# Performance work log

Measured on AMD Instinct MI355X. Metric: run time of the kernel, lower is better.

## Reference

```python
import jax, jax.numpy as jnp
import numpy as np

EMPTY = -1  # sentinel for empty (vertex, region) slots, as in the TF layer


def setup_inputs() -> dict:
    key = jax.random.key(0)
    m, vertices, regions = 128, 2048, 32
    # values in [-1, vertices): -1 marks an empty slot, otherwise a vertex id
    mapping = jax.random.randint(key, (m, vertices, regions), EMPTY, vertices, dtype=jnp.int32)
    return {"mapping": mapping}


def reference(mapping):
    """Faithful JAX version of Graph2Col.call.

    TF's tf.where(mask) emits coordinates of True entries in row-major order
    with a data-dependent row count. For jit-compatibility we emit a
    fixed-size [m*V*R, ...] result where valid entries come first (same
    row-major order as tf.where) and padding rows are filled with -1.
    """
    m, V, R = mapping.shape
    total = m * V * R
    flat_map = mapping.reshape(-1)                 # [total]
    # row index is never -1, so the reduce_all mask is simply mapping != -1
    flat_mask = flat_map != EMPTY                  # [total] bool

    # stable stream compaction: valid entries first, preserving row-major order
    order = jnp.argsort(~flat_mask)                # stable sort -> tf.where ordering
    valid = flat_mask[order]                       # [total] bool

    rows = order // (V * R)
    rem = order % (V * R)
    verts = rem // R
    regs = rem % R

    # column_indices: coordinates of non-empty slots (tf.where returns int64)
    column_indices = jnp.stack([rows, verts, regs], axis=-1).astype(jnp.int64)  # [total, 3]
    # nodes_indices: (batch_row, vertex_id) gathered at those coordinates (int32)
    nodes_indices = jnp.stack([rows.astype(jnp.int32), flat_map[order]], axis=-1)  # [total, 2]

    column_indices = jnp.where(valid[:, None], column_indices, jnp.int64(EMPTY))
    nodes_indices = jnp.where(valid[:, None], nodes_indices, jnp.int32(EMPTY))
    return nodes_indices, column_indices
```

## Files before the change

### kernel.cpp

```cpp
#include <hip/hip_runtime.h>


#define EMPTY_V (-1)

constexpr int M_DIM = 128;
constexpr int V_DIM = 2048;
constexpr int R_DIM = 32;
constexpr int TOTAL = M_DIM * V_DIM * R_DIM;
constexpr int BLOCK = 256;
constexpr int CHUNK = 8192;
constexpr int NB = TOTAL / CHUNK;
constexpr int SUBT = CHUNK / (BLOCK * 4);
constexpr int NWAVE = BLOCK / 64;
constexpr int STAGE = BLOCK * 4;

__global__ __launch_bounds__(BLOCK) void k_count(const int* __restrict__ in,
                                                 int* __restrict__ counts) {
    const int b = blockIdx.x;
    const int tid = threadIdx.x;
    const int4* p = (const int4*)(in + (size_t)b * CHUNK);
    int c = 0;
#pragma unroll
    for (int s = 0; s < SUBT; ++s) {
        int4 v = p[s * BLOCK + tid];
        c += (v.x != EMPTY_V) + (v.y != EMPTY_V) + (v.z != EMPTY_V) + (v.w != EMPTY_V);
    }
    for (int d = 32; d > 0; d >>= 1) c += __shfl_down(c, d, 64);
    __shared__ int ws[NWAVE];
    const int lane = tid & 63, wid = tid >> 6;
    if (lane == 0) ws[wid] = c;
    __syncthreads();
    if (tid == 0) {
        int t = 0;
        for (int w = 0; w < NWAVE; ++w) t += ws[w];
        counts[b] = t;
    }
}

__global__ __launch_bounds__(NB) void k_scan(const int* __restrict__ counts,
                                             int* __restrict__ offsets,
                                             int* __restrict__ total_valid) {
    const int tid = threadIdx.x;
    const int lane = tid & 63, wid = tid >> 6;
    int c = counts[tid];
    int incl = c;
    for (int d = 1; d < 64; d <<= 1) {
        int y = __shfl_up(incl, d, 64);
        if (lane >= d) incl += y;
    }
    __shared__ int ws[NB / 64];
    if (lane == 63) ws[wid] = incl;
    __syncthreads();
    int woff = 0;
    for (int w = 0; w < wid; ++w) woff += ws[w];
    offsets[tid] = woff + incl - c;
    if (tid == NB - 1) *total_valid = woff + incl;
}

__global__ __launch_bounds__(BLOCK) void k_scatter(const int* __restrict__ in,
                                                   const int* __restrict__ offsets,
                                                   int* __restrict__ out_nodes,
                                                   int* __restrict__ out_cols) {
    const int b = blockIdx.x;
    const int tid = threadIdx.x;
    const int lane = tid & 63, wid = tid >> 6;
    const unsigned long long below = lane ? ((~0ull) >> (64 - lane)) : 0ull;
    __shared__ int wsum[NWAVE];
    __shared__ int s_val[STAGE];
    __shared__ int s_pos[STAGE];
    const int row = b >> 3;
    int running = offsets[b];
    const int4* p = (const int4*)(in + (size_t)b * CHUNK);
#pragma unroll 1
    for (int s = 0; s < SUBT; ++s) {
        const int4 v = p[s * BLOCK + tid];
        const int f0 = (v.x != EMPTY_V), f1 = (v.y != EMPTY_V);
        const int f2 = (v.z != EMPTY_V), f3 = (v.w != EMPTY_V);
        const unsigned long long b0 = __ballot(f0), b1 = __ballot(f1);
        const unsigned long long b2 = __ballot(f2), b3 = __ballot(f3);
        const int pre = __popcll(b0 & below) + __popcll(b1 & below) +
                        __popcll(b2 & below) + __popcll(b3 & below);
        const int wtot = __popcll(b0) + __popcll(b1) + __popcll(b2) + __popcll(b3);
        if (lane == 0) wsum[wid] = wtot;
        __syncthreads();
        int woff = 0, cnt = 0;
        for (int w = 0; w < NWAVE; ++w) {
            const int x = wsum[w];
            cnt += x;
            if (w < wid) woff += x;
        }
        int lp = woff + pre;
        const int rem0 = ((b & 7) << 13) + (s << 10) + (tid << 2);
        const int vals[4] = {v.x, v.y, v.z, v.w};
        const int fl[4] = {f0, f1, f2, f3};
#pragma unroll
        for (int j = 0; j < 4; ++j) {
            if (fl[j]) { s_val[lp] = vals[j]; s_pos[lp] = rem0 + j; ++lp; }
        }
        __syncthreads();
        int2* ndst2 = (int2*)(out_nodes + 2 * (size_t)running);
        for (int k = tid; k < cnt; k += BLOCK) {
            ndst2[k] = make_int2(row, s_val[k]);
        }
        int* cdst = out_cols + 3 * (size_t)running;
        const int cdw = 3 * cnt;
        for (int d = tid; d < cdw; d += BLOCK) {
            const int e = d / 3;
            const int r = d - 3 * e;
            int val = row;
            if (r != 0) {
                const int pp = s_pos[e];
                val = (r == 1) ? (pp >> 5) : (pp & 31);
            }
            cdst[d] = val;
        }
        running += cnt;
        __syncthreads();
    }
}

__global__ __launch_bounds__(BLOCK) void k_tail(const int* __restrict__ total_valid,
                                                int* __restrict__ out_nodes,
                                                int* __restrict__ out_cols) {
    const int tv = *total_valid;
    const int stride = gridDim.x * blockDim.x;
    for (int pos = tv + blockIdx.x * blockDim.x + threadIdx.x; pos < TOTAL;
         pos += stride) {
        out_nodes[2 * pos]     = EMPTY_V;
        out_nodes[2 * pos + 1] = EMPTY_V;
        out_cols[3 * pos]      = EMPTY_V;
        out_cols[3 * pos + 1]  = EMPTY_V;
        out_cols[3 * pos + 2]  = EMPTY_V;
    }
}

extern "C" void kernel_launch(void* const* d_in, const int* in_sizes, int n_in,
                              void* d_out, int out_size, void* d_ws, size_t ws_size,
                              hipStream_t stream) {
    const int* in = (const int*)d_in[0];
    int* out = (int*)d_out;
    int* out_nodes = out;
    int* out_cols = out + 2 * (size_t)TOTAL;
    int* ws = (int*)d_ws;
    int* counts = ws;
    int* offsets = ws + NB;
    int* tv = ws + 2 * NB;

    k_count<<<NB, BLOCK, 0, stream>>>(in, counts);
    k_scan<<<1, NB, 0, stream>>>(counts, offsets, tv);
    k_scatter<<<NB, BLOCK, 0, stream>>>(in, offsets, out_nodes, out_cols);
    k_tail<<<512, BLOCK, 0, stream>>>(tv, out_nodes, out_cols);
}
```

Measured before the change: 196.7 us.

## Fold scan and tail fill into scatter kernel, vectorize output stores

Result: faster. 192.0 us (-2.4%).

```diff
diff --git a/kernel.cpp b/kernel.cpp
--- a/kernel.cpp
+++ b/kernel.cpp
@@ -37,39 +37,40 @@
     }
 }
 
-__global__ __launch_bounds__(NB) void k_scan(const int* __restrict__ counts,
-                                             int* __restrict__ offsets,
-                                             int* __restrict__ total_valid) {
-    const int tid = threadIdx.x;
-    const int lane = tid & 63, wid = tid >> 6;
-    int c = counts[tid];
-    int incl = c;
-    for (int d = 1; d < 64; d <<= 1) {
-        int y = __shfl_up(incl, d, 64);
-        if (lane >= d) incl += y;
-    }
-    __shared__ int ws[NB / 64];
-    if (lane == 63) ws[wid] = incl;
-    __syncthreads();
-    int woff = 0;
-    for (int w = 0; w < wid; ++w) woff += ws[w];
-    offsets[tid] = woff + incl - c;
-    if (tid == NB - 1) *total_valid = woff + incl;
-}
-
 __global__ __launch_bounds__(BLOCK) void k_scatter(const int* __restrict__ in,
-                                                   const int* __restrict__ offsets,
+                                                   const int* __restrict__ counts,
                                                    int* __restrict__ out_nodes,
                                                    int* __restrict__ out_cols) {
     const int b = blockIdx.x;
     const int tid = threadIdx.x;
     const int lane = tid & 63, wid = tid >> 6;
     const unsigned long long below = lane ? ((~0ull) >> (64 - lane)) : 0ull;
+
+    __shared__ int red[2 * NWAVE];
+    {
+        const int4 c4 = ((const int4*)counts)[tid];
+        const int idx0 = tid * 4;
+        const int cs[4] = {c4.x, c4.y, c4.z, c4.w};
+        int pa = 0, ta = 0;
+#pragma unroll
+        for (int j = 0; j < 4; ++j) {
+            ta += cs[j];
+            if (idx0 + j < b) pa += cs[j];
+        }
+        for (int d = 32; d > 0; d >>= 1) {
+            pa += __shfl_down(pa, d, 64);
+            ta += __shfl_down(ta, d, 64);
+        }
+        if (lane == 0) { red[wid] = pa; red[NWAVE + wid] = ta; }
+    }
+    __syncthreads();
+    int running = 0, tv = 0;
+    for (int w = 0; w < NWAVE; ++w) { running += red[w]; tv += red[NWAVE + w]; }
+
     __shared__ int wsum[NWAVE];
     __shared__ int s_val[STAGE];
     __shared__ int s_pos[STAGE];
     const int row = b >> 3;
-    int running = offsets[b];
     const int4* p = (const int4*)(in + (size_t)b * CHUNK);
 #pragma unroll 1
     for (int s = 0; s < SUBT; ++s) {
@@ -98,34 +99,62 @@
             if (fl[j]) { s_val[lp] = vals[j]; s_pos[lp] = rem0 + j; ++lp; }
         }
         __syncthreads();
-        int2* ndst2 = (int2*)(out_nodes + 2 * (size_t)running);
-        for (int k = tid; k < cnt; k += BLOCK) {
-            ndst2[k] = make_int2(row, s_val[k]);
+
+        {
+            int2* b2p = (int2*)out_nodes + running;
+            const int head = ((running & 1) && cnt > 0) ? 1 : 0;
+            if (head && tid == 0) b2p[0] = make_int2(row, s_val[0]);
+            const int nPairs = (cnt - head) >> 1;
+            int4* b4p = (int4*)(b2p + head);
+            for (int k = tid; k < nPairs; k += BLOCK) {
+                const int e = head + 2 * k;
+                b4p[k] = make_int4(row, s_val[e], row, s_val[e + 1]);
+            }
+            if (((cnt - head) & 1) && tid == BLOCK - 1)
+                b2p[cnt - 1] = make_int2(row, s_val[cnt - 1]);
         }
-        int* cdst = out_cols + 3 * (size_t)running;
-        const int cdw = 3 * cnt;
-        for (int d = tid; d < cdw; d += BLOCK) {
-            const int e = d / 3;
-            const int r = d - 3 * e;
-            int val = row;
-            if (r != 0) {
-                const int pp = s_pos[e];
-                val = (r == 1) ? (pp >> 5) : (pp & 31);
+        {
+            int* cd = out_cols + 3 * (size_t)running;
+            const int cdw = 3 * cnt;
+            const int mis = (3 * running) & 3;
+            int peel = mis ? (4 - mis) : 0;
+            if (peel > cdw) peel = cdw;
+            if (tid < peel) {
+                const int ld = tid;
+                const int e = ld / 3, r = ld - 3 * e;
+                int vv = row;
+                if (r) { const int pp = s_pos[e]; vv = (r == 1) ? (pp >> 5) : (pp & 31); }
+                cd[ld] = vv;
             }
-            cdst[d] = val;
+            const int body = (cdw - peel) >> 2;
+            int4* c4p = (int4*)(cd + peel);
+            for (int k = tid; k < body; k += BLOCK) {
+                const int ld0 = peel + 4 * k;
+                int vv[4];
+#pragma unroll
+                for (int i = 0; i < 4; ++i) {
+                    const int ld = ld0 + i;
+                    const int e = ld / 3, r = ld - 3 * e;
+                    int x = row;
+                    if (r) { const int pp = s_pos[e]; x = (r == 1) ? (pp >> 5) : (pp & 31); }
+                    vv[i] = x;
+                }
+                c4p[k] = make_int4(vv[0], vv[1], vv[2], vv[3]);
+            }
+            const int tails = cdw - peel - 4 * body;
+            if (tid < tails) {
+                const int ld = peel + 4 * body + tid;
+                const int e = ld / 3, r = ld - 3 * e;
+                int vv = row;
+                if (r) { const int pp = s_pos[e]; vv = (r == 1) ? (pp >> 5) : (pp & 31); }
+                cd[ld] = vv;
+            }
         }
         running += cnt;
         __syncthreads();
     }
-}
 
-__global__ __launch_bounds__(BLOCK) void k_tail(const int* __restrict__ total_valid,
-                                                int* __restrict__ out_nodes,
-                                                int* __restrict__ out_cols) {
-    const int tv = *total_valid;
-    const int stride = gridDim.x * blockDim.x;
-    for (int pos = tv + blockIdx.x * blockDim.x + threadIdx.x; pos < TOTAL;
-         pos += stride) {
+    for (int pos = tv + b * BLOCK + tid; pos < TOTAL; pos += NB * BLOCK) {
         out_nodes[2 * pos]     = EMPTY_V;
         out_nodes[2 * pos + 1] = EMPTY_V;
         out_cols[3 * pos]      = EMPTY_V;
@@ -141,13 +170,8 @@
     int* out = (int*)d_out;
     int* out_nodes = out;
     int* out_cols = out + 2 * (size_t)TOTAL;
-    int* ws = (int*)d_ws;
-    int* counts = ws;
-    int* offsets = ws + NB;
-    int* tv = ws + 2 * NB;
+    int* counts = (int*)d_ws;
 
     k_count<<<NB, BLOCK, 0, stream>>>(in, counts);
-    k_scan<<<1, NB, 0, stream>>>(counts, offsets, tv);
-    k_scatter<<<NB, BLOCK, 0, stream>>>(in, offsets, out_nodes, out_cols);
-    k_tail<<<512, BLOCK, 0, stream>>>(tv, out_nodes, out_cols);
+    k_scatter<<<NB, BLOCK, 0, stream>>>(in, counts, out_nodes, out_cols);
 }
```
